# Kernel optimization log

Measured on AMD Instinct MI355X. Metric: run time of the kernel, lower is better.

Reference implementation:

```python
import jax, jax.numpy as jnp
import numpy as np
import math

B, QL, KL, D, H, FF = 2, 2048, 2048, 512, 8, 2048
DH = D // H

def layernorm(x, g, b, eps=1e-5):
    m = jnp.mean(x, axis=-1, keepdims=True)
    v = jnp.mean((x - m) ** 2, axis=-1, keepdims=True)
    return (x - m) * jax.lax.rsqrt(v + eps) * g + b

def mha(x, mask, wq, bq, wk, bk, wv, bv, wo, bo, kv=None):
    # faithful port of MultiHeadAttention.forward (eval mode, dropout off)
    bs, qlen, dim = x.shape
    src = x if kv is None else kv
    def split(t):
        return t.reshape(bs, -1, H, DH).transpose(0, 2, 1, 3)  # [b,h,l,dh]
    q = split(x @ wq + bq) * (1.0 / math.sqrt(DH))
    k = split(src @ wk + bk)
    v = split(src @ wv + bv)
    scores = jnp.einsum('bhqd,bhkd->bhqk', q, k)
    m = mask[:, None, :, :] if mask.ndim == 3 else mask[:, None, None, :]
    scores = jnp.where(m == 0, -jnp.inf, scores)
    w = jax.nn.softmax(scores.astype(jnp.float32), axis=-1).astype(scores.dtype)
    ctx = jnp.einsum('bhqk,bhkd->bhqd', w, v)
    ctx = ctx.transpose(0, 2, 1, 3).reshape(bs, qlen, dim)
    return ctx @ wo + bo

def decoder_layer(tgt, memory, pos, tkpm, causal_mask, mem_mask,
                  sa, ca, l1w, l1b, l2w, l2b, n1g, n1b, n2g, n2b, n3g, n3b):
    tgt = tgt + pos
    t2 = layernorm(tgt, n1g, n1b)
    t2 = t2 * tkpm[:, :, None]
    t2 = mha(t2, causal_mask, *sa)
    tgt = tgt + t2
    t2 = layernorm(tgt, n2g, n2b)
    t2 = mha(t2, mem_mask, *ca, kv=memory)
    tgt = tgt + t2
    t2 = layernorm(tgt, n3g, n3b)
    t2 = jax.nn.relu(t2 @ l1w + l1b) @ l2w + l2b
    tgt = tgt + t2
    tgt = tgt * tkpm[:, :, None]
    return tgt

def setup_inputs() -> dict:
    key = jax.random.key(0)
    ks = jax.random.split(key, 32)
    it = iter(list(ks))
    def nrm(shape, s=0.02):
        return jax.random.normal(next(it), shape, jnp.float32) * s
    inp = {}
    inp['cfg'] = 0
    inp['tgt'] = jax.random.normal(next(it), (B, QL, D), jnp.float32)
    inp['memory'] = jax.random.normal(next(it), (B, KL, D), jnp.float32)
    inp['pos'] = jax.random.normal(next(it), (B, QL, D), jnp.float32)
    inp['causal_mask'] = jnp.broadcast_to(jnp.tril(jnp.ones((QL, QL), jnp.int32)), (B, QL, QL))
    inp['tgt_key_padding_mask'] = jnp.ones((B, QL), jnp.float32)
    mkpm = jax.random.randint(next(it), (B, KL), 0, 2).astype(jnp.int32)
    inp['memory_key_padding_mask'] = mkpm.at[:, 0].set(1)  # avoid fully-masked rows
    for p in ['sa', 'ca']:
        for w in ['q', 'k', 'v', 'o']:
            inp[f'{p}_{w}_w'] = nrm((D, D))
            inp[f'{p}_{w}_b'] = jnp.zeros((D,), jnp.float32)
    inp['lin1_w'] = nrm((D, FF)); inp['lin1_b'] = jnp.zeros((FF,), jnp.float32)
    inp['lin2_w'] = nrm((FF, D)); inp['lin2_b'] = jnp.zeros((D,), jnp.float32)
    for n in ['n1', 'n2', 'n3']:
        inp[f'{n}_g'] = jnp.ones((D,), jnp.float32)
        inp[f'{n}_b'] = jnp.zeros((D,), jnp.float32)
    return inp

def reference(cfg, tgt, memory, pos, causal_mask, tgt_key_padding_mask, memory_key_padding_mask,
              sa_q_w, sa_q_b, sa_k_w, sa_k_b, sa_v_w, sa_v_b, sa_o_w, sa_o_b,
              ca_q_w, ca_q_b, ca_k_w, ca_k_b, ca_v_w, ca_v_b, ca_o_w, ca_o_b,
              lin1_w, lin1_b, lin2_w, lin2_b,
              n1_g, n1_b, n2_g, n2_b, n3_g, n3_b):
    sa = (sa_q_w, sa_q_b, sa_k_w, sa_k_b, sa_v_w, sa_v_b, sa_o_w, sa_o_b)
    ca = (ca_q_w, ca_q_b, ca_k_w, ca_k_b, ca_v_w, ca_v_b, ca_o_w, ca_o_b)
    return decoder_layer(tgt, memory, pos, tgt_key_padding_mask, causal_mask, memory_key_padding_mask,
                         sa, ca, lin1_w, lin1_b, lin2_w, lin2_b, n1_g, n1_b, n2_g, n2_b, n3_g, n3_b)
```

## Files before the change

### kernel.cpp

```cpp
#include <hip/hip_runtime.h>
#include <hip/hip_bf16.h>
#include <stdint.h>

#define QL   2048
#define KLn  2048
#define DIM  512
#define NH   8
#define DH   64
#define NB   2
#define MROWS (NB*QL)
#define FFD  2048

typedef unsigned short u16;
typedef unsigned int u32;
typedef __attribute__((ext_vector_type(8))) short short8;
typedef __attribute__((ext_vector_type(4))) float f32x4;

__device__ __forceinline__ u16 f2b(float f){
  union { float f; u32 i; } v; v.f = f;
  u32 r = v.i + 0x7FFFu + ((v.i >> 16) & 1u);
  return (u16)(r >> 16);
}
__device__ __forceinline__ float b2f(u16 u){
  union { u32 i; float f; } v; v.i = ((u32)u) << 16; return v.f;
}
__device__ __forceinline__ u32 cvtpk(float a, float b){
  u32 r;
  asm("v_cvt_pk_bf16_f32 %0, %1, %2" : "=v"(r) : "v"(a), "v"(b));
  return r;
}

typedef __attribute__((address_space(3))) void as3void;
typedef __attribute__((address_space(1))) void as1void;
__device__ __forceinline__ void gload_lds16(const void* g, void* l){
  __builtin_amdgcn_global_load_lds((as1void*)g, (as3void*)l, 16, 0, 0);
}

#define BK 64
enum { EPI_BIAS=0, EPI_SCALEQ=1, EPI_RELU=2, EPI_RES=3, EPI_FIN=5, EPI_QKV=6, EPI_KV=7 };
#define QSCALE 0.1803368801111244f

template<int EPI>
__global__ __launch_bounds__(256, 4)
void gemm64(const u16* __restrict__ A, const u16* __restrict__ Bt,
            const float* __restrict__ bias,
            u16* __restrict__ Obf, float* __restrict__ Ores,
            const float* __restrict__ tk, float* __restrict__ fout,
            int K, int N)
{
  __shared__ __align__(16) u16 As[2][64*BK];
  __shared__ __align__(16) u16 Bs[2][64*BK];
  const int t  = threadIdx.x;
  const int l  = t & 63;
  const int lq = l & 15, lg = l >> 4;
  const int w  = t >> 6;
  const int wm = (w >> 1) * 32;
  const int wn = (w & 1) * 32;

  const int gx   = gridDim.x;
  const int nwg  = gx * gridDim.y;
  const int orig = blockIdx.x + gx * blockIdx.y;
  const int wgid = (orig & 7) * (nwg >> 3) + (orig >> 3);
  const int m0 = (wgid / gx) * 64;
  const int n0 = (wgid % gx) * 64;

  const int srow = t >> 3;
  const int scs  = t & 7;

  auto stageG = [&](u16* dA, u16* dB, int k0){
    _Pragma("unroll")
    for (int i = 0; i < 2; ++i){
      const int row = i*32 + srow;
      gload_lds16(A  + (size_t)(m0 + row)*K + k0 + ((scs ^ (row & 7)) << 3),
                  dA + row*BK + scs*8);
      gload_lds16(Bt + (size_t)(n0 + row)*K + k0 + ((scs ^ (row & 7)) << 3),
                  dB + row*BK + scs*8);
    }
  };

  int aoff[2][2], boff[2][2];
  _Pragma("unroll")
  for (int i = 0; i < 2; ++i)
    _Pragma("unroll")
    for (int kc = 0; kc < 2; ++kc){
      const int sw = (((kc*4 + lg) ^ (lq & 7)) << 3);
      aoff[i][kc] = ((wm + i*16 + lq)*BK + sw) * 2;
      boff[i][kc] = ((wn + i*16 + lq)*BK + sw) * 2;
    }

  f32x4 acc[2][2];
  _Pragma("unroll")
  for (int i=0;i<2;i++)
    _Pragma("unroll")
    for (int j=0;j<2;j++) acc[i][j] = (f32x4){0.f,0.f,0.f,0.f};

#define GBODY(BUF, KK)                                                        \
  {                                                                           \
    { const int ks = ((KK) + BK < K) ? (KK) + BK : 0;                         \
      stageG(As[(BUF)^1], Bs[(BUF)^1], ks); }                                 \
    asm volatile("s_waitcnt vmcnt(4)" ::: "memory");                          \
    __builtin_amdgcn_s_barrier();                                             \
    __builtin_amdgcn_sched_barrier(0);                                        \
    short8 af[2][2], bf[2][2];                                                \
    _Pragma("unroll")                                                         \
    for (int kc = 0; kc < 2; ++kc)                                            \
      _Pragma("unroll")                                                       \
      for (int i = 0; i < 2; ++i){                                            \
        af[i][kc] = *(const short8*)((const char*)As + (BUF)*8192 + aoff[i][kc]); \
        bf[i][kc] = *(const short8*)((const char*)Bs + (BUF)*8192 + boff[i][kc]); \
      }                                                                       \
    __builtin_amdgcn_s_barrier();                                             \
    __builtin_amdgcn_s_setprio(1);                                            \
    _Pragma("unroll")                                                         \
    for (int kc = 0; kc < 2; ++kc)                                            \
      _Pragma("unroll")                                                       \
      for (int i = 0; i < 2; ++i)                                             \
        _Pragma("unroll")                                                     \
        for (int j = 0; j < 2; ++j)                                           \
          acc[i][j] = __builtin_amdgcn_mfma_f32_16x16x32_bf16(af[i][kc], bf[j][kc], acc[i][j], 0,0,0); \
    __builtin_amdgcn_s_setprio(0);                                            \
  }

  stageG(As[0], Bs[0], 0);
  for (int k0 = 0; k0 < K; k0 += 2*BK){
    GBODY(0, k0)
    GBODY(1, k0 + BK)
  }
#undef GBODY

  _Pragma("unroll")
  for (int i=0;i<2;i++){
    _Pragma("unroll")
    for (int j=0;j<2;j++){
      _Pragma("unroll")
      for (int rr=0;rr<4;rr++){
        const int row = m0 + wm + i*16 + lg*4 + rr;
        const int col = n0 + wn + j*16 + lq;
        float v = acc[i][j][rr] + bias[col];
        if (EPI == EPI_SCALEQ) v *= QSCALE;
        if (EPI == EPI_RELU)   v = fmaxf(v, 0.f);
        if (EPI == EPI_RES)    Ores[(size_t)row*N + col] += v;
        else if (EPI == EPI_FIN){
          const size_t idx = (size_t)row*N + col;
          fout[idx] = (Ores[idx] + v) * tk[row];
        }
        else if (EPI == EPI_QKV){
          const int seg = col >> 9, c = col & 511;
          if (seg == 0)      Obf[(size_t)row*512 + c] = f2b(v * QSCALE);
          else if (seg == 1){
            const int bb = row >> 11, kv = row & 2047;
            const int hh = c >> 6,  dh = c & 63;
            Obf[(2u<<20) + ((((size_t)(bb*NH + hh) << 11) + kv) << 6) + (dh ^ ((kv & 7) << 3))] = f2b(v);
          }
          else               Obf[(4u<<20) + (size_t)row*512 + c] = f2b(v);
        }
        else if (EPI == EPI_KV){
          const int seg = col >> 9, c = col & 511;
          if (seg == 0){
            const int bb = row >> 11, kv = row & 2047;
            const int hh = c >> 6,  dh = c & 63;
            Obf[((((size_t)(bb*NH + hh) << 11) + kv) << 6) + (dh ^ ((kv & 7) << 3))] = f2b(v);
          }
          else               Obf[(2u<<20) + (size_t)row*512 + c] = f2b(v);
        }
        else                   Obf[(size_t)row*N + col] = f2b(v);
      }
    }
  }
}

__global__ __launch_bounds__(256, 4)
void gemm_om(const u16* __restrict__ ctxp, const float2* __restrict__ mlb,
             const u16* __restrict__ Bt, const float* __restrict__ bias,
             float* __restrict__ Ores)
{
  const int K = 512, N = 512;
  __shared__ __align__(16) u16 As[2][64*BK];
  __shared__ __align__(16) u16 Bs[2][64*BK];
  const int t  = threadIdx.x;
  const int l  = t & 63;
  const int lq = l & 15, lg = l >> 4;
  const int w  = t >> 6;
  const int wm = (w >> 1) * 32;
  const int wn = (w & 1) * 32;

  const int gx   = gridDim.x;
  const int nwg  = gx * gridDim.y;
  const int orig = blockIdx.x + gx * blockIdx.y;
  const int wgid = (orig & 7) * (nwg >> 3) + (orig >> 3);
  const int m0 = (wgid / gx) * 64;
  const int n0 = (wgid % gx) * 64;

  const int srow = t >> 3;
  const int scs  = t & 7;

  typedef __attribute__((ext_vector_type(4))) u32 u32x4;
  union Apack { u32x4 v; u16 e[8]; };

  auto loadA = [&](Apack* c0, Apack* c1, float2* a0, float2* a1, int k0){
    _Pragma("unroll")
    for (int i = 0; i < 2; ++i){
      const int row  = i*32 + srow;
      const int grow = m0 + row;
      const int b_   = grow >> 11, qr = grow & 2047;
      const int kk   = k0 + ((scs ^ (row & 7)) << 3);
      const int h_   = kk >> 6;
      c0[i].v = *(const u32x4*)&ctxp[(size_t)grow*512 + kk];
      c1[i].v = *(const u32x4*)&ctxp[(size_t)MROWS*512 + (size_t)grow*512 + kk];
      a0[i] = mlb[((size_t)(b_*NH + h_) << 11) + qr];
      a1[i] = mlb[((size_t)((NB + b_)*NH + h_) << 11) + qr];
    }
  };
  auto writeA = [&](u16* dA, Apack* c0, Apack* c1, float2* a0, float2* a1){
    _Pragma("unroll")
    for (int i = 0; i < 2; ++i){
      const int row = i*32 + srow;
      const float mg = fmaxf(a0[i].x, a1[i].x);
      const float w0 = exp2f(a0[i].x - mg), w1 = exp2f(a1[i].x - mg);
      const float rd = 1.f / (a0[i].y*w0 + a1[i].y*w1);
      u32x4 o;
      _Pragma("unroll")
      for (int j = 0; j < 4; ++j)
        o[j] = cvtpk((b2f(c0[i].e[2*j  ])*w0 + b2f(c1[i].e[2*j  ])*w1) * rd,
                     (b2f(c0[i].e[2*j+1])*w0 + b2f(c1[i].e[2*j+1])*w1) * rd);
      *(u32x4*)&dA[row*BK + scs*8] = o;
    }
  };
  auto stageB = [&](u16* dB, int k0){
    _Pragma("unroll")
    for (int i = 0; i < 2; ++i){
      const int row = i*32 + srow;
      gload_lds16(Bt + (size_t)(n0 + row)*K + k0 + ((scs ^ (row & 7)) << 3),
                  dB + row*BK + scs*8);
    }
  };

  int aoff[2][2], boff[2][2];
  _Pragma("unroll")
  for (int i = 0; i < 2; ++i)
    _Pragma("unroll")
    for (int kc = 0; kc < 2; ++kc){
      const int sw = (((kc*4 + lg) ^ (lq & 7)) << 3);
      aoff[i][kc] = ((wm + i*16 + lq)*BK + sw) * 2;
      boff[i][kc] = ((wn + i*16 + lq)*BK + sw) * 2;
    }

  f32x4 acc[2][2];
  _Pragma("unroll")
  for (int i=0;i<2;i++)
    _Pragma("unroll")
    for (int j=0;j<2;j++) acc[i][j] = (f32x4){0.f,0.f,0.f,0.f};

  {
    Apack c0[2], c1[2]; float2 a0[2], a1[2];
    loadA(c0, c1, a0, a1, 0);
    stageB(Bs[0], 0);
    writeA(As[0], c0, c1, a0, a1);
  }
  int cur = 0;
  for (int k0 = 0; k0 < K; k0 += BK){
    __syncthreads();
    short8 af[2][2], bf[2][2];
    _Pragma("unroll")
    for (int kc = 0; kc < 2; ++kc)
      _Pragma("unroll")
      for (int i = 0; i < 2; ++i){
        af[i][kc] = *(const short8*)((const char*)As + cur*8192 + aoff[i][kc]);
        bf[i][kc] = *(const short8*)((const char*)Bs + cur*8192 + boff[i][kc]);
      }
    __syncthreads();
    const bool has = (k0 + BK) < K;
    Apack c0[2], c1[2]; float2 a0[2], a1[2];
    if (has){
      loadA(c0, c1, a0, a1, k0 + BK);
      stageB(Bs[cur^1], k0 + BK);
    }
    __builtin_amdgcn_s_setprio(1);
    _Pragma("unroll")
    for (int kc = 0; kc < 2; ++kc)
      _Pragma("unroll")
      for (int i = 0; i < 2; ++i)
        _Pragma("unroll")
        for (int j = 0; j < 2; ++j)
          acc[i][j] = __builtin_amdgcn_mfma_f32_16x16x32_bf16(af[i][kc], bf[j][kc], acc[i][j], 0,0,0);
    __builtin_amdgcn_s_setprio(0);
    if (has) writeA(As[cur^1], c0, c1, a0, a1);
    cur ^= 1;
  }

  _Pragma("unroll")
  for (int i=0;i<2;i++){
    _Pragma("unroll")
    for (int j=0;j<2;j++){
      _Pragma("unroll")
      for (int rr=0;rr<4;rr++){
        const int row = m0 + wm + i*16 + lg*4 + rr;
        const int col = n0 + wn + j*16 + lq;
        Ores[(size_t)row*N + col] += acc[i][j][rr] + bias[col];
      }
    }
  }
}

template<bool CAUSAL>
__global__ __launch_bounds__(256, 2)
void attn8(const u16* __restrict__ Q, const u16* __restrict__ Kbh,
           const u16* __restrict__ Vth, const float* __restrict__ bias,
           u16* __restrict__ ctxp, float2* __restrict__ mlb)
{
  __shared__ __align__(16) u16 Kl[4][64*64];
  __shared__ __align__(16) u16 Vl[4][64*64];
  const int tid = threadIdx.x;
  const int l  = tid & 63;
  const int w  = tid >> 6;
  const int lq = l & 15, lg = l >> 4;
  const int h    = blockIdx.y;
  const int b    = blockIdx.z >> 1;
  const int half = blockIdx.z & 1;
  const int qtile = CAUSAL ? ((b & 1) ? (15 - (int)blockIdx.x) : (int)blockIdx.x)
                           : (int)blockIdx.x;
  const int rw = qtile*128 + w*32;

  const u16* kg = Kbh + ((size_t)(b*NH + h) << 17);
  const u16* vg = Vth + ((size_t)(b*NH + h) << 17);

  short8 aq[2][2];
  _Pragma("unroll")
  for (int g = 0; g < 2; ++g)
    _Pragma("unroll")
    for (int kc = 0; kc < 2; ++kc)
      aq[g][kc] = *(const short8*)(Q + (size_t)(b*QL + rw + g*16 + lq)*DIM + h*DH + kc*32 + lg*8);

  int koff[4][2];
  _Pragma("unroll")
  for (int j = 0; j < 4; ++j)
    _Pragma("unroll")
    for (int kc = 0; kc < 2; ++kc)
      koff[j][kc] = ((j*16 + lq)*64 + (((kc*4 + lg) ^ (lq & 7)) << 3)) * 2;

  f32x4 ctx[2][4];
  _Pragma("unroll")
  for (int g = 0; g < 2; ++g)
    _Pragma("unroll")
    for (int d = 0; d < 4; ++d) ctx[g][d] = (f32x4){0.f,0.f,0.f,0.f};
  f32x4 ls0 = (f32x4){0.f,0.f,0.f,0.f};
  f32x4 ls1 = (f32x4){0.f,0.f,0.f,0.f};
  float m0v = -1e30f, m1v = -1e30f;

  const int ntiles = CAUSAL ? (2*qtile + 2) : (KLn >> 6);
  const int P = (ntiles > half) ? ((ntiles - half + 1) >> 1) : 0;

  auto stageA = [&](u16* dK, u16* dV, int tile){
    const u16* kgs = kg + ((size_t)tile << 12);
    const u16* vgs = vg + tile*64;
    gload_lds16(kgs + w*1024 + l*8,       dK + w*1024 + l*8);
    gload_lds16(kgs + w*1024 + 512 + l*8, dK + w*1024 + 512 + l*8);
    gload_lds16(vgs + (size_t)(w*16 +     (l>>3))*KLn + (l&7)*8, dV + w*1024 + l*8);
    gload_lds16(vgs + (size_t)(w*16 + 8 + (l>>3))*KLn + (l&7)*8, dV + w*1024 + 512 + l*8);
  };

#define ABODY(BUF, II)                                                        \
  {                                                                           \
    const int TT = half + 2*(II);                                             \
    f32x4 bv[4];                                                              \
    if (!CAUSAL){                                                             \
      _Pragma("unroll")                                                       \
      for (int sub = 0; sub < 4; ++sub)                                       \
        bv[sub] = *(const f32x4*)(bias + b*KLn + TT*64 + sub*16 + lg*4);      \
    }                                                                         \
    { const int i2 = (II) + 2;                                                \
      const int ts = (i2 < P) ? half + 2*i2 : half;                           \
      stageA(Kl[((BUF)+2)&3], Vl[((BUF)+2)&3], ts); }                         \
    if (CAUSAL) asm volatile("s_waitcnt vmcnt(8)" ::: "memory");              \
    else        asm volatile("s_waitcnt vmcnt(12)" ::: "memory");             \
    __builtin_amdgcn_s_barrier();                                             \
    __builtin_amdgcn_sched_barrier(0);                                        \
    f32x4 s[2][4];                                                            \
    _Pragma("unroll")                                                         \
    for (int g = 0; g < 2; ++g)                                               \
      _Pragma("unroll")                                                       \
      for (int sub = 0; sub < 4; ++sub) s[g][sub] = (f32x4){0.f,0.f,0.f,0.f}; \
    _Pragma("unroll")                                                         \
    for (int sub = 0; sub < 4; ++sub)                                         \
      _Pragma("unroll")                                                       \
      for (int kc = 0; kc < 2; ++kc){                                         \
        short8 bk = *(const short8*)((const char*)Kl + (BUF)*8192 + koff[sub][kc]); \
        s[0][sub] = __builtin_amdgcn_mfma_f32_16x16x32_bf16(bk, aq[0][kc], s[0][sub], 0,0,0); \
        s[1][sub] = __builtin_amdgcn_mfma_f32_16x16x32_bf16(bk, aq[1][kc], s[1][sub], 0,0,0); \
      }                                                                       \
    if (CAUSAL){                                                              \
      if (TT*64 + 63 > rw){                                                   \
        _Pragma("unroll")                                                     \
        for (int g = 0; g < 2; ++g)                                           \
          _Pragma("unroll")                                                   \
          for (int sub = 0; sub < 4; ++sub)                                   \
            _Pragma("unroll")                                                 \
            for (int rr = 0; rr < 4; ++rr)                                    \
              if (TT*64 + sub*16 + lg*4 + rr > rw + g*16 + lq) s[g][sub][rr] = -1e30f; \
      }                                                                       \
    } else {                                                                  \
      _Pragma("unroll")                                                       \
      for (int g = 0; g < 2; ++g)                                             \
        _Pragma("unroll")                                                     \
        for (int sub = 0; sub < 4; ++sub) s[g][sub] += bv[sub];               \
    }                                                                         \
    float px0 = s[0][0][0], px1 = s[1][0][0];                                 \
    _Pragma("unroll")                                                         \
    for (int sub = 0; sub < 4; ++sub)                                         \
      _Pragma("unroll")                                                       \
      for (int rr = 0; rr < 4; ++rr){                                         \
        px0 = fmaxf(px0, s[0][sub][rr]);                                      \
        px1 = fmaxf(px1, s[1][sub][rr]);                                      \
      }                                                                       \
    if (!__all(px0 <= m0v + 8.0f && px1 <= m1v + 8.0f)){                      \
      px0 = fmaxf(px0, __shfl_xor(px0, 16));                                  \
      px0 = fmaxf(px0, __shfl_xor(px0, 32));                                  \
      px1 = fmaxf(px1, __shfl_xor(px1, 16));                                  \
      px1 = fmaxf(px1, __shfl_xor(px1, 32));                                  \
      const float mn0 = fmaxf(m0v, px0), mn1 = fmaxf(m1v, px1);               \
      const float c0 = exp2f(m0v - mn0), c1 = exp2f(m1v - mn1);               \
      ls0 *= c0; ls1 *= c1;                                                   \
      _Pragma("unroll")                                                       \
      for (int rr = 0; rr < 4; ++rr){                                         \
        const float b0 = __shfl(c0, lg*4 + rr), b1 = __shfl(c1, lg*4 + rr);   \
        _Pragma("unroll")                                                     \
        for (int d = 0; d < 4; ++d){ ctx[0][d][rr] *= b0; ctx[1][d][rr] *= b1; } \
      }                                                                       \
      m0v = mn0; m1v = mn1;                                                   \
    }                                                                         \
    u32 pk0[4][2], pk1[4][2];                                                 \
    _Pragma("unroll")                                                         \
    for (int sub = 0; sub < 4; ++sub){                                        \
      float a0 = exp2f(s[0][sub][0] - m0v), a1 = exp2f(s[0][sub][1] - m0v);   \
      float a2 = exp2f(s[0][sub][2] - m0v), a3 = exp2f(s[0][sub][3] - m0v);   \
      ls0 += (f32x4){a0, a1, a2, a3};                                         \
      pk0[sub][0] = cvtpk(a0, a1); pk0[sub][1] = cvtpk(a2, a3);               \
      float e0 = exp2f(s[1][sub][0] - m1v), e1 = exp2f(s[1][sub][1] - m1v);   \
      float e2 = exp2f(s[1][sub][2] - m1v), e3 = exp2f(s[1][sub][3] - m1v);   \
      ls1 += (f32x4){e0, e1, e2, e3};                                         \
      pk1[sub][0] = cvtpk(e0, e1); pk1[sub][1] = cvtpk(e2, e3);               \
    }                                                                         \
    union { u32 u[4]; short8 s8; } pA0, pA1, pB0, pB1;                        \
    pA0.u[0] = pk0[0][0]; pA0.u[1] = pk0[0][1]; pA0.u[2] = pk0[1][0]; pA0.u[3] = pk0[1][1]; \
    pA1.u[0] = pk0[2][0]; pA1.u[1] = pk0[2][1]; pA1.u[2] = pk0[3][0]; pA1.u[3] = pk0[3][1]; \
    pB0.u[0] = pk1[0][0]; pB0.u[1] = pk1[0][1]; pB0.u[2] = pk1[1][0]; pB0.u[3] = pk1[1][1]; \
    pB1.u[0] = pk1[2][0]; pB1.u[1] = pk1[2][1]; pB1.u[2] = pk1[3][0]; pB1.u[3] = pk1[3][1]; \
    _Pragma("unroll")                                                         \
    for (int d0 = 0; d0 < 4; ++d0){                                           \
      short8 v0 = *(const short8*)((const char*)Vl + (BUF)*8192 + koff[d0][0]); \
      short8 v1 = *(const short8*)((const char*)Vl + (BUF)*8192 + koff[d0][1]); \
      ctx[0][d0] = __builtin_amdgcn_mfma_f32_16x16x32_bf16(pA0.s8, v0, ctx[0][d0], 0,0,0); \
      ctx[0][d0] = __builtin_amdgcn_mfma_f32_16x16x32_bf16(pA1.s8, v1, ctx[0][d0], 0,0,0); \
      ctx[1][d0] = __builtin_amdgcn_mfma_f32_16x16x32_bf16(pB0.s8, v0, ctx[1][d0], 0,0,0); \
      ctx[1][d0] = __builtin_amdgcn_mfma_f32_16x16x32_bf16(pB1.s8, v1, ctx[1][d0], 0,0,0); \
    }                                                                         \
    __builtin_amdgcn_s_barrier();                                             \
  }

  if (P > 0){
    stageA(Kl[0], Vl[0], half);
    { const int ts1 = (1 < P) ? half + 2 : half;
      stageA(Kl[1], Vl[1], ts1); }
    for (int i = 0; i < P; i += 4){
      ABODY(0, i)
      if (i + 1 < P) ABODY(1, i + 1)
      if (i + 2 < P) ABODY(2, i + 2)
      if (i + 3 < P) ABODY(3, i + 3)
    }
  }
#undef ABODY

  float h0 = (ls0[0] + ls0[1]) + (ls0[2] + ls0[3]);
  float h1 = (ls1[0] + ls1[1]) + (ls1[2] + ls1[3]);
  h0 += __shfl_xor(h0, 16); h0 += __shfl_xor(h0, 32);
  h1 += __shfl_xor(h1, 16); h1 += __shfl_xor(h1, 32);
  if (lg == 0){
    mlb[((size_t)((half*NB + b)*NH + h) << 11) + rw + lq]      = make_float2(m0v, h0);
    mlb[((size_t)((half*NB + b)*NH + h) << 11) + rw + 16 + lq] = make_float2(m1v, h1);
  }
  u16* cp = ctxp + (size_t)half*MROWS*DIM;
  _Pragma("unroll")
  for (int g = 0; g < 2; ++g)
    _Pragma("unroll")
    for (int d0 = 0; d0 < 4; ++d0)
      _Pragma("unroll")
      for (int rr = 0; rr < 4; ++rr)
        cp[(size_t)(b*QL + rw + g*16 + lg*4 + rr)*DIM + h*DH + d0*16 + lq] =
            f2b(ctx[g][d0][rr]);
}

template<int MODE>
__global__ __launch_bounds__(128)
void ln_kernel(const float* __restrict__ in0, const float* __restrict__ in1,
               const float* __restrict__ tkpm,
               const float* __restrict__ g, const float* __restrict__ bvec,
               float* __restrict__ xres, u16* __restrict__ outb)
{
  const int row = blockIdx.x;
  const int t = threadIdx.x;
  float v[4];
  #pragma unroll
  for (int i = 0; i < 4; ++i){
    const int c = t + i*128;
    float x = in0[(size_t)row*DIM + c];
    if (MODE == 0){
      x += in1[(size_t)row*DIM + c];
      xres[(size_t)row*DIM + c] = x;
    }
    v[i] = x;
  }
  float s = v[0]+v[1]+v[2]+v[3];
  #pragma unroll
  for (int off = 1; off < 64; off <<= 1) s += __shfl_xor(s, off);
  __shared__ float red[4];
  if ((t & 63) == 0) red[t >> 6] = s;
  __syncthreads();
  const float mean = (red[0] + red[1]) * (1.f/512.f);
  float q = 0.f;
  #pragma unroll
  for (int i = 0; i < 4; ++i){ const float d = v[i]-mean; q += d*d; }
  #pragma unroll
  for (int off = 1; off < 64; off <<= 1) q += __shfl_xor(q, off);
  if ((t & 63) == 0) red[2 + (t >> 6)] = q;
  __syncthreads();
  const float var = (red[2] + red[3]) * (1.f/512.f);
  const float rs = rsqrtf(var + 1e-5f);
  const float tk = (MODE == 0) ? tkpm[row] : 1.f;
  #pragma unroll
  for (int i = 0; i < 4; ++i){
    const int c = t + i*128;
    const float y = (v[i] - mean) * rs * g[c] + bvec[c];
    outb[(size_t)row*DIM + c] = f2b(y * tk);
  }
}

__global__ __launch_bounds__(256)
void prep_all(const float* w0, const float* w1, const float* w2, const float* w3,
              const float* w4, const float* w5, const float* w6, const float* w7,
              const float* __restrict__ mem, const int* __restrict__ mkpm,
              const float* saqb, const float* sakb, const float* savb,
              const float* cakb, const float* cavb,
              u16* __restrict__ wtA, u16* __restrict__ memb,
              float* __restrict__ bias, float* __restrict__ bc0,
              float* __restrict__ bc1)
{
  __shared__ float tile[32][33];
  const int id = blockIdx.x;
  const int tid = threadIdx.x;
  if (id < 2048){
    const int z = id >> 8, rem = id & 255;
    const int r0 = (rem >> 4) * 32, c0 = (rem & 15) * 32;
    const float* wp[8] = {w0,w1,w2,w3,w4,w5,w6,w7};
    const float* w = wp[z];
    u16* o = wtA + (size_t)z * 512 * 512;
    const int tx = tid & 31, ty = tid >> 5;
    #pragma unroll
    for (int i = 0; i < 4; ++i)
      tile[ty + i*8][tx] = w[(size_t)(r0 + ty + i*8)*512 + c0 + tx];
    __syncthreads();
    #pragma unroll
    for (int i = 0; i < 4; ++i)
      o[(size_t)(c0 + ty + i*8)*512 + r0 + tx] = f2b(tile[tx][ty + i*8]);
  } else if (id < 4096){
    const int i = (id - 2048)*1024 + tid*4;
    f32x4 v = *(const f32x4*)&mem[i];
    uint2 p; p.x = cvtpk(v[0], v[1]); p.y = cvtpk(v[2], v[3]);
    *(uint2*)&memb[i] = p;
  } else {
    const int j = (id - 4096)*256 + tid;
    bias[j] = mkpm[j] ? 0.f : -1e30f;
    if (j < 1536) bc0[j] = (j < 512) ? saqb[j] : (j < 1024) ? sakb[j-512] : savb[j-1024];
    if (j < 1024) bc1[j] = (j < 512) ? cakb[j] : cavb[j-512];
  }
}

__global__ __launch_bounds__(256)
void transpose_vperm(const u16* __restrict__ in, u16* __restrict__ out)
{
  __shared__ u16 tile[32][33];
  in  += (size_t)blockIdx.z * KLn * DIM;
  out += (size_t)blockIdx.z * NH * DH * KLn;
  const int tx = threadIdx.x, ty = threadIdx.y;
  const int r0 = blockIdx.y*32, c0 = blockIdx.x*32;
  #pragma unroll
  for (int i = 0; i < 4; ++i)
    tile[ty + i*8][tx] = in[(size_t)(r0 + ty + i*8)*DIM + c0 + tx];
  __syncthreads();
  const int kv = r0 + tx;
  const int s  = (kv & ~31) | (((kv>>2)&3)<<3) | (((kv>>4)&1)<<2) | (kv&3);
  #pragma unroll
  for (int i = 0; i < 4; ++i){
    const int dcol = c0 + ty + i*8;
    const int hh = dcol >> 6, dh = dcol & 63;
    const int kvpos = (s & ~63) | (((((s>>3)&7) ^ (dh&7)) << 3)) | (s & 7);
    out[((size_t)(hh*DH + dh))*KLn + kvpos] = tile[tx][ty + i*8];
  }
}

__global__ __launch_bounds__(256)
void prep_cross(const u16* __restrict__ vb, u16* __restrict__ vt,
                const float* __restrict__ l1w, u16* __restrict__ l1wt,
                const float* __restrict__ l2w, u16* __restrict__ l2wt)
{
  const int id = blockIdx.x;
  const int tid = threadIdx.x;
  const int tx = tid & 31, ty = tid >> 5;
  if (id < 2048){
    __shared__ u16 tileu[32][33];
    const int z = id >> 10, rem = id & 1023;
    const int c0 = (rem & 15) * 32, r0 = (rem >> 4) * 32;
    const u16* in = vb + (size_t)z * KLn * DIM;
    u16* out = vt + (size_t)z * NH * DH * KLn;
    #pragma unroll
    for (int i = 0; i < 4; ++i)
      tileu[ty + i*8][tx] = in[(size_t)(r0 + ty + i*8)*DIM + c0 + tx];
    __syncthreads();
    const int kv = r0 + tx;
    const int s  = (kv & ~31) | (((kv>>2)&3)<<3) | (((kv>>4)&1)<<2) | (kv&3);
    #pragma unroll
    for (int i = 0; i < 4; ++i){
      const int dcol = c0 + ty + i*8;
      const int hh = dcol >> 6, dh = dcol & 63;
      const int kvpos = (s & ~63) | (((((s>>3)&7) ^ (dh&7)) << 3)) | (s & 7);
      out[((size_t)(hh*DH + dh))*KLn + kvpos] = tileu[tx][ty + i*8];
    }
  } else {
    __shared__ float tilef[32][33];
    if (id < 3072){
      const int rem = id - 2048;
      const int c0 = (rem & 63) * 32, r0 = (rem >> 6) * 32;
      #pragma unroll
      for (int i = 0; i < 4; ++i)
        tilef[ty + i*8][tx] = l1w[(size_t)(r0 + ty + i*8)*FFD + c0 + tx];
      __syncthreads();
      #pragma unroll
      for (int i = 0; i < 4; ++i)
        l1wt[(size_t)(c0 + ty + i*8)*512 + r0 + tx] = f2b(tilef[tx][ty + i*8]);
    } else {
      const int rem = id - 3072;
      const int c0 = (rem & 15) * 32, r0 = (rem >> 4) * 32;
      #pragma unroll
      for (int i = 0; i < 4; ++i)
        tilef[ty + i*8][tx] = l2w[(size_t)(r0 + ty + i*8)*512 + c0 + tx];
      __syncthreads();
      #pragma unroll
      for (int i = 0; i < 4; ++i)
        l2wt[(size_t)(c0 + ty + i*8)*FFD + r0 + tx] = f2b(tilef[tx][ty + i*8]);
    }
  }
}

extern "C" void kernel_launch(void* const* d_in, const int* in_sizes, int n_in,
                              void* d_out, int out_size, void* d_ws, size_t ws_size,
                              hipStream_t stream)
{
  const float* tgt  = (const float*)d_in[1];
  const float* mem  = (const float*)d_in[2];
  const float* pos  = (const float*)d_in[3];
  const float* tkpm = (const float*)d_in[5];
  const int*   mkpm = (const int*)d_in[6];
  const float* saqw = (const float*)d_in[7];  const float* saqb = (const float*)d_in[8];
  const float* sakw = (const float*)d_in[9];  const float* sakb = (const float*)d_in[10];
  const float* savw = (const float*)d_in[11]; const float* savb = (const float*)d_in[12];
  const float* saow = (const float*)d_in[13]; const float* saob = (const float*)d_in[14];
  const float* caqw = (const float*)d_in[15]; const float* caqb = (const float*)d_in[16];
  const float* cakw = (const float*)d_in[17]; const float* cakb = (const float*)d_in[18];
  const float* cavw = (const float*)d_in[19]; const float* cavb = (const float*)d_in[20];
  const float* caow = (const float*)d_in[21]; const float* caob = (const float*)d_in[22];
  const float* l1w  = (const float*)d_in[23]; const float* l1b  = (const float*)d_in[24];
  const float* l2w  = (const float*)d_in[25]; const float* l2b  = (const float*)d_in[26];
  const float* n1g  = (const float*)d_in[27]; const float* n1b  = (const float*)d_in[28];
  const float* n2g  = (const float*)d_in[29]; const float* n2b  = (const float*)d_in[30];
  const float* n3g  = (const float*)d_in[31]; const float* n3b  = (const float*)d_in[32];

  if (ws_size < 58720256) return;

  char* ws = (char*)d_ws;
  float* xres = (float*)(ws);
  u16* t2n    = (u16*)(ws + (8u<<20));
  u16* qb     = (u16*)(ws + (12u<<20));
  u16* kb     = (u16*)(ws + (16u<<20));
  u16* vb     = (u16*)(ws + (20u<<20));
  u16* vt     = (u16*)(ws + (24u<<20));
  float* bias = (float*)(ws + (28u<<20));
  float* bc0  = (float*)(ws + (28u<<20) + 16384);
  float* bc1  = (float*)(ws + (28u<<20) + 24576);
  float2* mlb = (float2*)(ws + (28u<<20) + 32768);
  u16* l1wt   = (u16*)(ws + (29u<<20));
  u16* l2wt   = (u16*)(ws + (31u<<20));
  u16* memb   = (u16*)(ws + (33u<<20));
  u16* wtA    = (u16*)(ws + (37u<<20));
  u16* ctxp   = (u16*)(ws + (41u<<20));
  u16* ffh    = (u16*)(ws + (12u<<20));

  float* out = (float*)d_out;
  const int W55 = 512*512;

  prep_all<<<dim3(4112), 256, 0, stream>>>(saqw, sakw, savw, saow,
                                           caqw, cakw, cavw, caow,
                                           mem, mkpm, saqb, sakb, savb, cakb, cavb,
                                           wtA, memb, bias, bc0, bc1);
  ln_kernel<0><<<MROWS, 128, 0, stream>>>(tgt, pos, tkpm, n1g, n1b, xres, t2n);

  #define G(EP, GX) gemm64<EP><<<dim3(GX,64), 256, 0, stream>>>

  G(EPI_QKV, 24)(t2n, wtA, bc0, qb, nullptr, nullptr, nullptr, 512, 1536);
  transpose_vperm<<<dim3(DIM/32, KLn/32, NB), dim3(32,8), 0, stream>>>(vb, vt);
  attn8<true><<<dim3(QL/128, NH, NB*2), 256, 0, stream>>>(qb, kb, vt, nullptr, ctxp, mlb);
  gemm_om<<<dim3(8,64), 256, 0, stream>>>(ctxp, mlb, wtA + 3*W55, saob, xres);

  ln_kernel<1><<<MROWS, 128, 0, stream>>>(xres, nullptr, nullptr, n2g, n2b, nullptr, t2n);

  G(EPI_SCALEQ, 8)(t2n,  wtA + 4*W55, caqb, qb, nullptr, nullptr, nullptr, 512, 512);
  G(EPI_KV, 16)(memb, wtA + 5*W55, bc1, kb, nullptr, nullptr, nullptr, 512, 1024);
  prep_cross<<<dim3(4096), 256, 0, stream>>>(vb, vt, l1w, l1wt, l2w, l2wt);
  attn8<false><<<dim3(QL/128, NH, NB*2), 256, 0, stream>>>(qb, kb, vt, bias, ctxp, mlb);
  gemm_om<<<dim3(8,64), 256, 0, stream>>>(ctxp, mlb, wtA + 7*W55, caob, xres);

  ln_kernel<1><<<MROWS, 128, 0, stream>>>(xres, nullptr, nullptr, n3g, n3b, nullptr, t2n);

  G(EPI_RELU, 32)(t2n, l1wt, l1b, ffh, nullptr, nullptr, nullptr, 512, FFD);
  G(EPI_FIN, 8)(ffh, l2wt, l2b, nullptr, xres, tkpm, out, 2048, 512);

  #undef G
}
```

Before: 190.1 us.

## Split attention KV range three ways with double-buffered LDS and higher occupancy

Attention now splits each query tile's key range across three workgroups instead of two, and the output-projection GEMM merges three partial contexts using their max/sum statistics. The K/V LDS ring shrinks from four to two buffers, and launch bounds ask for three blocks per CU, so more workgroups can be resident and the grid grows by half. The aim is better CU utilisation, especially for the uneven causal work. The costs are more partial-context traffic and merge arithmetic, and a shallower prefetch depth that may expose load latency. The statistics buffer is moved to a new workspace offset to make room.

```diff
diff --git a/kernel.cpp b/kernel.cpp
--- a/kernel.cpp
+++ b/kernel.cpp
@@ -10,6 +10,7 @@
 #define NB   2
 #define MROWS (NB*QL)
 #define FFD  2048
+#define NSPLIT 3
 
 typedef unsigned short u16;
 typedef unsigned int u32;
@@ -197,7 +198,7 @@
   typedef __attribute__((ext_vector_type(4))) u32 u32x4;
   union Apack { u32x4 v; u16 e[8]; };
 
-  auto loadA = [&](Apack* c0, Apack* c1, float2* a0, float2* a1, int k0){
+  auto loadA = [&](Apack (*c)[NSPLIT], float2 (*a)[NSPLIT], int k0){
     _Pragma("unroll")
     for (int i = 0; i < 2; ++i){
       const int row  = i*32 + srow;
@@ -205,24 +206,35 @@
       const int b_   = grow >> 11, qr = grow & 2047;
       const int kk   = k0 + ((scs ^ (row & 7)) << 3);
       const int h_   = kk >> 6;
-      c0[i].v = *(const u32x4*)&ctxp[(size_t)grow*512 + kk];
-      c1[i].v = *(const u32x4*)&ctxp[(size_t)MROWS*512 + (size_t)grow*512 + kk];
-      a0[i] = mlb[((size_t)(b_*NH + h_) << 11) + qr];
-      a1[i] = mlb[((size_t)((NB + b_)*NH + h_) << 11) + qr];
+      _Pragma("unroll")
+      for (int s = 0; s < NSPLIT; ++s){
+        c[i][s].v = *(const u32x4*)&ctxp[(size_t)s*MROWS*512 + (size_t)grow*512 + kk];
+        a[i][s] = mlb[((size_t)((s*NB + b_)*NH + h_) << 11) + qr];
+      }
     }
   };
-  auto writeA = [&](u16* dA, Apack* c0, Apack* c1, float2* a0, float2* a1){
+  auto writeA = [&](u16* dA, Apack (*c)[NSPLIT], float2 (*a)[NSPLIT]){
     _Pragma("unroll")
     for (int i = 0; i < 2; ++i){
       const int row = i*32 + srow;
-      const float mg = fmaxf(a0[i].x, a1[i].x);
-      const float w0 = exp2f(a0[i].x - mg), w1 = exp2f(a1[i].x - mg);
-      const float rd = 1.f / (a0[i].y*w0 + a1[i].y*w1);
+      float mg = a[i][0].x;
+      _Pragma("unroll")
+      for (int s = 1; s < NSPLIT; ++s) mg = fmaxf(mg, a[i][s].x);
+      float ws[NSPLIT], den = 0.f;
+      _Pragma("unroll")
+      for (int s = 0; s < NSPLIT; ++s){ ws[s] = exp2f(a[i][s].x - mg); den += a[i][s].y * ws[s]; }
+      const float rd = 1.f / den;
       u32x4 o;
       _Pragma("unroll")
-      for (int j = 0; j < 4; ++j)
-        o[j] = cvtpk((b2f(c0[i].e[2*j  ])*w0 + b2f(c1[i].e[2*j  ])*w1) * rd,
-                     (b2f(c0[i].e[2*j+1])*w0 + b2f(c1[i].e[2*j+1])*w1) * rd);
+      for (int j = 0; j < 4; ++j){
+        float lo = 0.f, hi = 0.f;
+        _Pragma("unroll")
+        for (int s = 0; s < NSPLIT; ++s){
+          lo += b2f(c[i][s].e[2*j  ]) * ws[s];
+          hi += b2f(c[i][s].e[2*j+1]) * ws[s];
+        }
+        o[j] = cvtpk(lo * rd, hi * rd);
+      }
       *(u32x4*)&dA[row*BK + scs*8] = o;
     }
   };
@@ -252,10 +264,10 @@
     for (int j=0;j<2;j++) acc[i][j] = (f32x4){0.f,0.f,0.f,0.f};
 
   {
-    Apack c0[2], c1[2]; float2 a0[2], a1[2];
-    loadA(c0, c1, a0, a1, 0);
+    Apack c[2][NSPLIT]; float2 a[2][NSPLIT];
+    loadA(c, a, 0);
     stageB(Bs[0], 0);
-    writeA(As[0], c0, c1, a0, a1);
+    writeA(As[0], c, a);
   }
   int cur = 0;
   for (int k0 = 0; k0 < K; k0 += BK){
@@ -270,9 +282,9 @@
       }
     __syncthreads();
     const bool has = (k0 + BK) < K;
-    Apack c0[2], c1[2]; float2 a0[2], a1[2];
+    Apack c[2][NSPLIT]; float2 a[2][NSPLIT];
     if (has){
-      loadA(c0, c1, a0, a1, k0 + BK);
+      loadA(c, a, k0 + BK);
       stageB(Bs[cur^1], k0 + BK);
     }
     __builtin_amdgcn_s_setprio(1);
@@ -284,7 +296,7 @@
         for (int j = 0; j < 2; ++j)
           acc[i][j] = __builtin_amdgcn_mfma_f32_16x16x32_bf16(af[i][kc], bf[j][kc], acc[i][j], 0,0,0);
     __builtin_amdgcn_s_setprio(0);
-    if (has) writeA(As[cur^1], c0, c1, a0, a1);
+    if (has) writeA(As[cur^1], c, a);
     cur ^= 1;
   }
 
@@ -303,20 +315,20 @@
 }
 
 template<bool CAUSAL>
-__global__ __launch_bounds__(256, 2)
-void attn8(const u16* __restrict__ Q, const u16* __restrict__ Kbh,
+__global__ __launch_bounds__(256, 3)
+void attn9(const u16* __restrict__ Q, const u16* __restrict__ Kbh,
            const u16* __restrict__ Vth, const float* __restrict__ bias,
            u16* __restrict__ ctxp, float2* __restrict__ mlb)
 {
-  __shared__ __align__(16) u16 Kl[4][64*64];
-  __shared__ __align__(16) u16 Vl[4][64*64];
+  __shared__ __align__(16) u16 Kl[2][64*64];
+  __shared__ __align__(16) u16 Vl[2][64*64];
   const int tid = threadIdx.x;
   const int l  = tid & 63;
   const int w  = tid >> 6;
   const int lq = l & 15, lg = l >> 4;
-  const int h    = blockIdx.y;
-  const int b    = blockIdx.z >> 1;
-  const int half = blockIdx.z & 1;
+  const int h     = blockIdx.y;
+  const int b     = blockIdx.z & 1;
+  const int split = blockIdx.z >> 1;
   const int qtile = CAUSAL ? ((b & 1) ? (15 - (int)blockIdx.x) : (int)blockIdx.x)
                            : (int)blockIdx.x;
   const int rw = qtile*128 + w*32;
@@ -348,7 +360,7 @@
   float m0v = -1e30f, m1v = -1e30f;
 
   const int ntiles = CAUSAL ? (2*qtile + 2) : (KLn >> 6);
-  const int P = (ntiles > half) ? ((ntiles - half + 1) >> 1) : 0;
+  const int P = (ntiles > split) ? ((ntiles - split + 2) / 3) : 0;
 
   auto stageA = [&](u16* dK, u16* dV, int tile){
     const u16* kgs = kg + ((size_t)tile << 12);
@@ -361,18 +373,18 @@
 
 #define ABODY(BUF, II)                                                        \
   {                                                                           \
-    const int TT = half + 2*(II);                                             \
+    const int TT = split + 3*(II);                                            \
     f32x4 bv[4];                                                              \
     if (!CAUSAL){                                                             \
       _Pragma("unroll")                                                       \
       for (int sub = 0; sub < 4; ++sub)                                       \
         bv[sub] = *(const f32x4*)(bias + b*KLn + TT*64 + sub*16 + lg*4);      \
     }                                                                         \
-    { const int i2 = (II) + 2;                                                \
-      const int ts = (i2 < P) ? half + 2*i2 : half;                           \
-      stageA(Kl[((BUF)+2)&3], Vl[((BUF)+2)&3], ts); }                         \
-    if (CAUSAL) asm volatile("s_waitcnt vmcnt(8)" ::: "memory");              \
-    else        asm volatile("s_waitcnt vmcnt(12)" ::: "memory");             \
+    { const int i2 = (II) + 1;                                                \
+      const int ts = (i2 < P) ? split + 3*i2 : split;                         \
+      stageA(Kl[(BUF)^1], Vl[(BUF)^1], ts); }                                 \
+    if (CAUSAL) asm volatile("s_waitcnt vmcnt(4)" ::: "memory");              \
+    else        asm volatile("s_waitcnt vmcnt(8)" ::: "memory");              \
     __builtin_amdgcn_s_barrier();                                             \
     __builtin_amdgcn_sched_barrier(0);                                        \
     f32x4 s[2][4];                                                            \
@@ -458,14 +470,10 @@
   }
 
   if (P > 0){
-    stageA(Kl[0], Vl[0], half);
-    { const int ts1 = (1 < P) ? half + 2 : half;
-      stageA(Kl[1], Vl[1], ts1); }
-    for (int i = 0; i < P; i += 4){
+    stageA(Kl[0], Vl[0], split);
+    for (int i = 0; i < P; i += 2){
       ABODY(0, i)
       if (i + 1 < P) ABODY(1, i + 1)
-      if (i + 2 < P) ABODY(2, i + 2)
-      if (i + 3 < P) ABODY(3, i + 3)
     }
   }
 #undef ABODY
@@ -475,10 +483,10 @@
   h0 += __shfl_xor(h0, 16); h0 += __shfl_xor(h0, 32);
   h1 += __shfl_xor(h1, 16); h1 += __shfl_xor(h1, 32);
   if (lg == 0){
-    mlb[((size_t)((half*NB + b)*NH + h) << 11) + rw + lq]      = make_float2(m0v, h0);
-    mlb[((size_t)((half*NB + b)*NH + h) << 11) + rw + 16 + lq] = make_float2(m1v, h1);
-  }
-  u16* cp = ctxp + (size_t)half*MROWS*DIM;
+    mlb[((size_t)((split*NB + b)*NH + h) << 11) + rw + lq]      = make_float2(m0v, h0);
+    mlb[((size_t)((split*NB + b)*NH + h) << 11) + rw + 16 + lq] = make_float2(m1v, h1);
+  }
+  u16* cp = ctxp + (size_t)split*MROWS*DIM;
   _Pragma("unroll")
   for (int g = 0; g < 2; ++g)
     _Pragma("unroll")
@@ -685,12 +693,12 @@
   float* bias = (float*)(ws + (28u<<20));
   float* bc0  = (float*)(ws + (28u<<20) + 16384);
   float* bc1  = (float*)(ws + (28u<<20) + 24576);
-  float2* mlb = (float2*)(ws + (28u<<20) + 32768);
   u16* l1wt   = (u16*)(ws + (29u<<20));
   u16* l2wt   = (u16*)(ws + (31u<<20));
   u16* memb   = (u16*)(ws + (33u<<20));
   u16* wtA    = (u16*)(ws + (37u<<20));
   u16* ctxp   = (u16*)(ws + (41u<<20));
+  float2* mlb = (float2*)(ws + (53u<<20));
   u16* ffh    = (u16*)(ws + (12u<<20));
 
   float* out = (float*)d_out;
@@ -706,7 +714,7 @@
 
   G(EPI_QKV, 24)(t2n, wtA, bc0, qb, nullptr, nullptr, nullptr, 512, 1536);
   transpose_vperm<<<dim3(DIM/32, KLn/32, NB), dim3(32,8), 0, stream>>>(vb, vt);
-  attn8<true><<<dim3(QL/128, NH, NB*2), 256, 0, stream>>>(qb, kb, vt, nullptr, ctxp, mlb);
+  attn9<true><<<dim3(QL/128, NH, NB*NSPLIT), 256, 0, stream>>>(qb, kb, vt, nullptr, ctxp, mlb);
   gemm_om<<<dim3(8,64), 256, 0, stream>>>(ctxp, mlb, wtA + 3*W55, saob, xres);
 
   ln_kernel<1><<<MROWS, 128, 0, stream>>>(xres, nullptr, nullptr, n2g, n2b, nullptr, t2n);
@@ -714,7 +722,7 @@
   G(EPI_SCALEQ, 8)(t2n,  wtA + 4*W55, caqb, qb, nullptr, nullptr, nullptr, 512, 512);
   G(EPI_KV, 16)(memb, wtA + 5*W55, bc1, kb, nullptr, nullptr, nullptr, 512, 1024);
   prep_cross<<<dim3(4096), 256, 0, stream>>>(vb, vt, l1w, l1wt, l2w, l2wt);
-  attn8<false><<<dim3(QL/128, NH, NB*2), 256, 0, stream>>>(qb, kb, vt, bias, ctxp, mlb);
+  attn9<false><<<dim3(QL/128, NH, NB*NSPLIT), 256, 0, stream>>>(qb, kb, vt, bias, ctxp, mlb);
   gemm_om<<<dim3(8,64), 256, 0, stream>>>(ctxp, mlb, wtA + 7*W55, caob, xres);
 
   ln_kernel<1><<<MROWS, 128, 0, stream>>>(xres, nullptr, nullptr, n3g, n3b, nullptr, t2n);
```

Result: slower. 200.0 us (+5.2%).
